# Kernel optimization log

Hardware: AMD Instinct MI355X
Metric: run time of the kernel (lower is better)

The kernel has to match this reference:

```python
import jax, jax.numpy as jnp
import numpy as np

MARGIN = 0.2
LAMBDA_SOFTMAX = 9.0
LAMBDA_LSE = 6.0
WEIGHT_FACTOR = 0.7  # attn_prev is absent/zero on the i2t path
EPS = 1e-8
NEG_INF = -1e9


def setup_inputs() -> dict:
    key = jax.random.key(0)
    k1, k2, k3 = jax.random.split(key, 3)
    B, R, W, D = 128, 36, 32, 256  # batch, regions, max words, feat dim
    im = jax.random.normal(k1, (B, R, D), jnp.float32)
    s = jax.random.normal(k2, (B, W, D), jnp.float32)
    s_l = jax.random.randint(k3, (B,), 1, W + 1)  # caption lengths in [1, W]
    return {"im": im, "s": s, "s_l": s_l}


def _xattn_scores_i2t(im, s, s_l):
    # im: (B, R, D) images; s: (C, W, D) captions; s_l: (C,) lengths
    C, W = s.shape[0], s.shape[1]
    word_mask = jnp.arange(W)[None, :] < s_l[:, None]  # (C, W)

    # func_attention(query=images, context=caption words):
    # attn[c,b,w,r] = <s[c,w], im[b,r]>
    attn = jnp.einsum('cwd,brd->cbwr', s, im)
    # raw_feature_norm == 'clipped_l2norm': LeakyReLU(0.1) then l2norm over region axis
    attn = jax.nn.leaky_relu(attn, 0.1)
    attn = attn / (jnp.sqrt(jnp.sum(attn * attn, axis=-1, keepdims=True)) + EPS)
    # softmax over sourceL = words, with smoothing; mask padded words
    logits = jnp.where(word_mask[:, None, :, None], attn * LAMBDA_SOFTMAX, NEG_INF)
    A = jax.nn.softmax(logits, axis=2)  # (C, B, W, R), sums to 1 over words
    # weightedContext[c,b,r,:] = 0.7 * sum_w A[c,b,w,r] * s[c,w,:]
    wC = WEIGHT_FACTOR * jnp.einsum('cbwr,cwd->cbrd', A, s)

    # cosine similarity between image regions and weighted caption context
    num = jnp.sum(im[None] * wC, axis=-1)                      # (C, B, R)
    denom = jnp.linalg.norm(im, axis=-1)[None] * jnp.linalg.norm(wC, axis=-1)
    row_sim = num / jnp.clip(denom, EPS)

    # agg_func == 'LogSumExp' over regions
    sim = jax.nn.logsumexp(LAMBDA_LSE * row_sim, axis=2) / LAMBDA_LSE  # (C, B)
    return sim.T  # scores: (n_image, n_caption)


def reference(im, s, s_l):
    scores = _xattn_scores_i2t(im, s, s_l)
    diag = jnp.diag(scores)
    cost_s = jnp.clip(MARGIN + scores - diag[:, None], 0.0)   # caption retrieval
    cost_im = jnp.clip(MARGIN + scores - diag[None, :], 0.0)  # image retrieval
    eye = jnp.eye(scores.shape[0], dtype=bool)
    cost_s = jnp.where(eye, 0.0, cost_s)
    cost_im = jnp.where(eye, 0.0, cost_im)
    # max_violation=True: hardest negatives
    return jnp.sum(jnp.max(cost_s, axis=1)) + jnp.sum(jnp.max(cost_im, axis=0))
```

## Files before the change

### kernel.cpp

```cpp
#include <hip/hip_runtime.h>
#include <math.h>

#define CN 128
#define RN 36
#define WN 32
#define DN 256

#define SSTR  264
#define GSTR  40
#define ATSTR 40

#define WS_SCORES 0
#define WS_SF    65536
#define WS_IMF   (WS_SF + CN*16384)
#define WS_TAILF (WS_IMF + CN*16384)
#define WS_G     (WS_TAILF + CN*8192)
#define WS_N2I   (WS_G + CN*2048)
#define WS_NEED  (WS_N2I + CN*RN*4)

typedef unsigned short u16;
typedef __attribute__((ext_vector_type(4))) unsigned short u16x4;
typedef __attribute__((ext_vector_type(8))) unsigned short u16x8;
typedef __attribute__((ext_vector_type(8))) __bf16 bf16x8;
typedef __attribute__((ext_vector_type(4))) float f32x4;

#define C9   12.9842502f
#define C6   8.65616798f
#define IC6  0.115524530f

__device__ __forceinline__ float bf2f(u16 u){ return __uint_as_float(((unsigned)u)<<16); }
__device__ __forceinline__ u16 f2bf(float f){ unsigned x=__float_as_uint(f); return (u16)((x + 0x7fffu + ((x>>16)&1u))>>16); }
__device__ __forceinline__ u16 f2bf_hw(float f){ __bf16 h = (__bf16)f; return __builtin_bit_cast(u16, h); }
__device__ __forceinline__ float lrelu(float v){ return fmaxf(v, 0.1f*v); }

__device__ __forceinline__ void gload16(const void* g, void* l){
    __builtin_amdgcn_global_load_lds((const __attribute__((address_space(1))) void*)g,
                                     (__attribute__((address_space(3))) void*)l, 16, 0, 0);
}

__global__ __launch_bounds__(256)
void precompute_kernel(const float* __restrict__ im, const float* __restrict__ s,
                       char* __restrict__ ws)
{
    const int tid = threadIdx.x;
    if (blockIdx.x < 128) {
        const int i = blockIdx.x;
        __shared__ __align__(16) u16 s_lds[WN*SSTR];
        __shared__ __align__(16) u16 g_lds[WN*GSTR];
        const float* src = s + (size_t)i*(WN*DN);
        u16* outf = (u16*)(ws + WS_SF) + (size_t)i*8192;
#pragma unroll
        for (int it = 0; it < 4; it++) {
            int idx = tid + it*256;
            int m = idx >> 9, ks = (idx >> 6) & 7, ln = idx & 63;
            int cc = ln & 15, gg = ln >> 4;
            const float4* p = (const float4*)(src + (m*16+cc)*DN + ks*32 + gg*8);
            float4 v0 = p[0], v1 = p[1];
            u16x8 hh = { f2bf_hw(v0.x),f2bf_hw(v0.y),f2bf_hw(v0.z),f2bf_hw(v0.w),
                         f2bf_hw(v1.x),f2bf_hw(v1.y),f2bf_hw(v1.z),f2bf_hw(v1.w) };
            *(u16x8*)(outf + (size_t)idx*8) = hh;
            *(u16x8*)&s_lds[(m*16+cc)*SSTR + ks*32 + gg*8] = hh;
        }
        __syncthreads();
        {
            const int lane = tid & 63, wv = tid >> 6;
            const int cc = lane & 15, gg = lane >> 4;
            const int gm = wv >> 1, gn = wv & 1;
            f32x4 acc = {0.f,0.f,0.f,0.f};
#pragma unroll
            for (int ks = 0; ks < 8; ks++) {
                int k0 = ks*32 + gg*8;
                bf16x8 a  = *(const bf16x8*)&s_lds[(gm*16+cc)*SSTR + k0];
                bf16x8 bb = *(const bf16x8*)&s_lds[(gn*16+cc)*SSTR + k0];
                acc = __builtin_amdgcn_mfma_f32_16x16x32_bf16(a, bb, acc, 0, 0, 0);
            }
            u16x4 hg = { f2bf_hw(acc[0]), f2bf_hw(acc[1]), f2bf_hw(acc[2]), f2bf_hw(acc[3]) };
            *(u16x4*)&g_lds[(gn*16+cc)*GSTR + gm*16 + gg*4] = hg;
        }
        __syncthreads();
        if (tid < 128) {
            int t = tid >> 6, ln = tid & 63;
            int cc = ln & 15, gg = ln >> 4;
            u16x8 gv = *(const u16x8*)&g_lds[(t*16+cc)*GSTR + gg*8];
            *(u16x8*)((u16*)(ws + WS_G) + (size_t)i*1024 + tid*8) = gv;
        }
    } else {
        const int i = blockIdx.x - 128;
        const float* src = im + (size_t)i*(RN*DN);
        u16* outf = (u16*)(ws + WS_IMF) + (size_t)i*8192;
#pragma unroll
        for (int it = 0; it < 4; it++) {
            int idx = tid + it*256;
            int m = idx >> 9, ks = (idx >> 6) & 7, ln = idx & 63;
            int cc = ln & 15, gg = ln >> 4;
            const float4* p = (const float4*)(src + (m*16+cc)*DN + ks*32 + gg*8);
            float4 v0 = p[0], v1 = p[1];
            u16x8 hh = { f2bf_hw(v0.x),f2bf_hw(v0.y),f2bf_hw(v0.z),f2bf_hw(v0.w),
                         f2bf_hw(v1.x),f2bf_hw(v1.y),f2bf_hw(v1.z),f2bf_hw(v1.w) };
            *(u16x8*)(outf + (size_t)idx*8) = hh;
        }
        u16* tout = (u16*)(ws + WS_TAILF) + (size_t)i*4096;
#pragma unroll
        for (int it = 0; it < 2; it++) {
            int idx = tid + it*256;
            int ks = idx >> 6, ln = idx & 63;
            int cc = ln & 15, gg = ln >> 4;
            int trow = (cc > 3) ? 3 : cc;
            const float4* p = (const float4*)(src + (32+trow)*DN + ks*32 + gg*8);
            float4 v0 = p[0], v1 = p[1];
            u16x8 hh = { f2bf_hw(v0.x),f2bf_hw(v0.y),f2bf_hw(v0.z),f2bf_hw(v0.w),
                         f2bf_hw(v1.x),f2bf_hw(v1.y),f2bf_hw(v1.z),f2bf_hw(v1.w) };
            *(u16x8*)(tout + (size_t)idx*8) = hh;
        }
        float* n2o = (float*)(ws + WS_N2I) + (size_t)i*RN;
#pragma unroll
        for (int it = 0; it < 2; it++) {
            int idx = tid + it*256;
            if (idx < 288) {
                int r = idx >> 3, q = idx & 7;
                const float4* p = (const float4*)(src + r*DN + q*32);
                float ss = 0.f;
#pragma unroll
                for (int k = 0; k < 8; k++) {
                    float4 v = p[k];
                    ss = fmaf(v.x,v.x,ss); ss = fmaf(v.y,v.y,ss);
                    ss = fmaf(v.z,v.z,ss); ss = fmaf(v.w,v.w,ss);
                }
                ss += __shfl_xor(ss,1); ss += __shfl_xor(ss,2); ss += __shfl_xor(ss,4);
                if (q == 0) n2o[r] = ss;
            }
        }
    }
}

__global__ __launch_bounds__(512, 3)
void xattn_staged(const int* __restrict__ s_l, char* __restrict__ ws)
{
    __shared__ __align__(16) u16 at_all[8*48*ATSTR];

    const int tid = threadIdx.x;
    const int lane = tid & 63, wv = tid >> 6;
    const int bq = blockIdx.x, cp = blockIdx.y;
    const int ci = wv >> 2, bi = wv & 3;
    const int c = cp*2 + ci, b = bq*4 + bi;
    const int col = lane & 15, g4 = lane >> 4;
    const int L = s_l[c];
    const int r2c = (32+col > 35) ? 35 : 32+col;

    const char* sf  = ws + WS_SF    + (size_t)c*16384;
    const char* mf  = ws + WS_IMF   + (size_t)b*16384;
    const char* tf  = ws + WS_TAILF + (size_t)b*8192;
    const char* gfp = ws + WS_G     + (size_t)c*2048;

    bf16x8 gf0 = *(const bf16x8*)(gfp + lane*16);
    bf16x8 gf1 = *(const bf16x8*)(gfp + 1024 + lane*16);
    const float* n2p = (const float*)(ws + WS_N2I) + (size_t)b*RN;
    float n2v0 = n2p[col];
    float n2v1 = n2p[16+col];
    float n2v2 = n2p[r2c];

    f32x4 raw[2][3];
#pragma unroll
    for (int m = 0; m < 2; m++)
#pragma unroll
        for (int n = 0; n < 3; n++) raw[m][n] = (f32x4){0.f,0.f,0.f,0.f};

#pragma unroll
    for (int ks = 0; ks < 8; ks++) {
        bf16x8 a0 = *(const bf16x8*)(sf +        ks*1024 + lane*16);
        bf16x8 a1 = *(const bf16x8*)(sf + 8192 + ks*1024 + lane*16);
        bf16x8 b0 = *(const bf16x8*)(mf +        ks*1024 + lane*16);
        bf16x8 b1 = *(const bf16x8*)(mf + 8192 + ks*1024 + lane*16);
        bf16x8 b2 = *(const bf16x8*)(tf +        ks*1024 + lane*16);
        raw[0][0] = __builtin_amdgcn_mfma_f32_16x16x32_bf16(a0, b0, raw[0][0], 0,0,0);
        raw[0][1] = __builtin_amdgcn_mfma_f32_16x16x32_bf16(a0, b1, raw[0][1], 0,0,0);
        raw[0][2] = __builtin_amdgcn_mfma_f32_16x16x32_bf16(a0, b2, raw[0][2], 0,0,0);
        raw[1][0] = __builtin_amdgcn_mfma_f32_16x16x32_bf16(a1, b0, raw[1][0], 0,0,0);
        raw[1][1] = __builtin_amdgcn_mfma_f32_16x16x32_bf16(a1, b1, raw[1][1], 0,0,0);
        raw[1][2] = __builtin_amdgcn_mfma_f32_16x16x32_bf16(a1, b2, raw[1][2], 0,0,0);
    }

    float af[2][3][4];
#pragma unroll
    for (int m = 0; m < 2; m++) {
#pragma unroll
        for (int reg = 0; reg < 4; reg++) {
            float ssum = 0.f;
#pragma unroll
            for (int n = 0; n < 3; n++) {
                float v = lrelu(raw[m][n][reg]);
                if (n == 2 && col >= 4) v = 0.f;
                af[m][n][reg] = v;
                ssum = fmaf(v, v, ssum);
            }
            ssum += __shfl_xor(ssum, 1);
            ssum += __shfl_xor(ssum, 2);
            ssum += __shfl_xor(ssum, 4);
            ssum += __shfl_xor(ssum, 8);
            float inv2 = C9 / (sqrtf(ssum) + 1e-8f);
#pragma unroll
            for (int n = 0; n < 3; n++) af[m][n][reg] *= inv2;
        }
    }

    float num[3];
#pragma unroll
    for (int n = 0; n < 3; n++) {
        float nm = 0.f;
#pragma unroll
        for (int m = 0; m < 2; m++)
#pragma unroll
            for (int reg = 0; reg < 4; reg++) {
                int w = m*16 + g4*4 + reg;
                float e = (w < L) ? __builtin_amdgcn_exp2f(af[m][n][reg]) : 0.f;
                af[m][n][reg] = e;
                nm = fmaf(e, raw[m][n][reg], nm);
            }
        nm += __shfl_xor(nm, 16);
        nm += __shfl_xor(nm, 32);
        num[n] = nm;
    }

    u16* at = at_all + wv*1920;
#pragma unroll
    for (int m = 0; m < 2; m++)
#pragma unroll
        for (int n = 0; n < 3; n++) {
            u16x4 h = { f2bf_hw(af[m][n][0]), f2bf_hw(af[m][n][1]),
                        f2bf_hw(af[m][n][2]), f2bf_hw(af[m][n][3]) };
            *(u16x4*)&at[(n*16 + col)*ATSTR + m*16 + g4*4] = h;
        }

    float qv[3];
#pragma unroll
    for (int n = 0; n < 3; n++) {
        bf16x8 bfv = *(const bf16x8*)&at[(n*16 + col)*ATSTR + g4*8];
        f32x4 z = {0.f,0.f,0.f,0.f};
        f32x4 t0 = __builtin_amdgcn_mfma_f32_16x16x32_bf16(gf0, bfv, z, 0,0,0);
        f32x4 t1 = __builtin_amdgcn_mfma_f32_16x16x32_bf16(gf1, bfv, z, 0,0,0);
        float q = 0.f;
#pragma unroll
        for (int reg = 0; reg < 4; reg++) {
            q = fmaf(af[0][n][reg], t0[reg], q);
            q = fmaf(af[1][n][reg], t1[reg], q);
        }
        q += __shfl_xor(q, 16);
        q += __shfl_xor(q, 32);
        qv[n] = q;
    }

    float es = 0.f;
#pragma unroll
    for (int n = 0; n < 3; n++) {
        float n2a = (n == 0) ? n2v0 : (n == 1) ? n2v1 : n2v2;
        float rs = num[n] * rsqrtf(fmaxf(n2a * qv[n], 1e-16f));
        bool valid = (n < 2) || (col < 4);
        if (valid) es += __builtin_amdgcn_exp2f(C6 * rs);
    }
    es += __shfl_xor(es, 1);
    es += __shfl_xor(es, 2);
    es += __shfl_xor(es, 4);
    es += __shfl_xor(es, 8);

    if (lane == 0)
        ((float*)(ws + WS_SCORES))[(size_t)b * CN + c] =
            __builtin_amdgcn_logf(es) * IC6;
}

__global__ __launch_bounds__(512, 2)
void xattn_fallback(const float* __restrict__ im, const float* __restrict__ s,
                    const int* __restrict__ s_l, float* __restrict__ scores)
{
    __shared__ u16   s_lds[2][WN*SSTR];
    __shared__ u16   im_lds[4][RN*SSTR];
    __shared__ u16   g_lds[2][WN*GSTR];
    __shared__ u16   at_lds[8][48*ATSTR];
    __shared__ float n2i_lds[4][RN];

    const int tid  = threadIdx.x;
    const int lane = tid & 63;
    const int wv   = tid >> 6;
    const int bq   = blockIdx.x, cp = blockIdx.y;
    const int ci   = wv >> 2, bi = wv & 3;
    const int c    = cp*2 + ci, b = bq*4 + bi;
    const int col  = lane & 15, g4 = lane >> 4;

    if (wv < 4) {
        const float4* g = (const float4*)(im + (size_t)(bq*4 + wv) * (RN*DN));
        u16* dst = im_lds[wv];
#pragma unroll
        for (int k = 0; k < 36; k++) {
            int i = lane + k*64;
            float4 v = g[i];
            int row = i >> 6, cc = (i & 63) * 4;
            u16x4 h = { f2bf(v.x), f2bf(v.y), f2bf(v.z), f2bf(v.w) };
            *(u16x4*)&dst[row*SSTR + cc] = h;
        }
    } else {
        int cap = (wv - 4) >> 1;
        int l2  = ((wv - 4) & 1) * 64 + lane;
        const float4* g = (const float4*)(s + (size_t)(cp*2 + cap) * (WN*DN));
        u16* dst = s_lds[cap];
#pragma unroll
        for (int k = 0; k < 16; k++) {
            int i = l2 + k*128;
            float4 v = g[i];
            int row = i >> 6, cc = (i & 63) * 4;
            u16x4 h = { f2bf(v.x), f2bf(v.y), f2bf(v.z), f2bf(v.w) };
            *(u16x4*)&dst[row*SSTR + cc] = h;
        }
    }
    __syncthreads();

    {
        const int gm = (wv >> 1) & 1, gn = wv & 1;
        const u16* sb = s_lds[ci];
        f32x4 acc = {0.f, 0.f, 0.f, 0.f};
#pragma unroll
        for (int ks = 0; ks < 8; ks++) {
            int k0 = ks*32 + g4*8;
            bf16x8 af = *(const bf16x8*)&sb[(gm*16 + col)*SSTR + k0];
            bf16x8 bfv = *(const bf16x8*)&sb[(gn*16 + col)*SSTR + k0];
            acc = __builtin_amdgcn_mfma_f32_16x16x32_bf16(af, bfv, acc, 0, 0, 0);
        }
        u16x4 h = { f2bf(acc[0]), f2bf(acc[1]), f2bf(acc[2]), f2bf(acc[3]) };
        *(u16x4*)&g_lds[ci][(gn*16 + col)*GSTR + gm*16 + g4*4] = h;
    }

    if (wv < 4) {
        const u16* ib = im_lds[wv];
        int r = lane >> 1, half = lane & 1;
        float ss = 0.f;
        const u16x8* p = (const u16x8*)&ib[r*SSTR + half*128];
#pragma unroll
        for (int k = 0; k < 16; k++) {
            u16x8 v = p[k];
#pragma unroll
            for (int j = 0; j < 8; j++) { float f = bf2f(v[j]); ss = fmaf(f, f, ss); }
        }
        ss += __shfl_xor(ss, 1);
        if (half == 0) n2i_lds[wv][r] = ss;
        if (lane < 8) {
            int r2 = 32 + (lane >> 1), h2 = lane & 1;
            float s2 = 0.f;
            const u16x8* p2 = (const u16x8*)&ib[r2*SSTR + h2*128];
#pragma unroll
            for (int k = 0; k < 16; k++) {
                u16x8 v = p2[k];
#pragma unroll
                for (int j = 0; j < 8; j++) { float f = bf2f(v[j]); s2 = fmaf(f, f, s2); }
            }
            s2 += __shfl_xor(s2, 1);
            if (h2 == 0) n2i_lds[wv][r2] = s2;
        }
    }

    const u16* sb = s_lds[ci];
    const u16* ib = im_lds[bi];
    f32x4 raw[2][3];
#pragma unroll
    for (int m = 0; m < 2; m++)
#pragma unroll
        for (int n = 0; n < 3; n++) raw[m][n] = (f32x4){0.f,0.f,0.f,0.f};
    {
        int r2c = 32 + col; if (r2c > 35) r2c = 35;
#pragma unroll
        for (int ks = 0; ks < 8; ks++) {
            int k0 = ks*32 + g4*8;
            bf16x8 a0 = *(const bf16x8*)&sb[col*SSTR + k0];
            bf16x8 a1 = *(const bf16x8*)&sb[(16 + col)*SSTR + k0];
            bf16x8 b0 = *(const bf16x8*)&ib[col*SSTR + k0];
            bf16x8 b1 = *(const bf16x8*)&ib[(16 + col)*SSTR + k0];
            bf16x8 b2 = *(const bf16x8*)&ib[r2c*SSTR + k0];
            raw[0][0] = __builtin_amdgcn_mfma_f32_16x16x32_bf16(a0, b0, raw[0][0], 0,0,0);
            raw[0][1] = __builtin_amdgcn_mfma_f32_16x16x32_bf16(a0, b1, raw[0][1], 0,0,0);
            raw[0][2] = __builtin_amdgcn_mfma_f32_16x16x32_bf16(a0, b2, raw[0][2], 0,0,0);
            raw[1][0] = __builtin_amdgcn_mfma_f32_16x16x32_bf16(a1, b0, raw[1][0], 0,0,0);
            raw[1][1] = __builtin_amdgcn_mfma_f32_16x16x32_bf16(a1, b1, raw[1][1], 0,0,0);
            raw[1][2] = __builtin_amdgcn_mfma_f32_16x16x32_bf16(a1, b2, raw[1][2], 0,0,0);
        }
    }

    float af[2][3][4];
#pragma unroll
    for (int m = 0; m < 2; m++) {
#pragma unroll
        for (int reg = 0; reg < 4; reg++) {
            float ssum = 0.f;
#pragma unroll
            for (int n = 0; n < 3; n++) {
                float v = lrelu(raw[m][n][reg]);
                if (n == 2 && col >= 4) v = 0.f;
                af[m][n][reg] = v;
                ssum = fmaf(v, v, ssum);
            }
            ssum += __shfl_xor(ssum, 1);
            ssum += __shfl_xor(ssum, 2);
            ssum += __shfl_xor(ssum, 4);
            ssum += __shfl_xor(ssum, 8);
            float inv = 1.0f / (sqrtf(ssum) + 1e-8f);
#pragma unroll
            for (int n = 0; n < 3; n++) af[m][n][reg] *= inv;
        }
    }

    const int L = s_l[c];
    float num[3], qv[3];
#pragma unroll
    for (int n = 0; n < 3; n++) {
        float mx = -1e30f;
#pragma unroll
        for (int m = 0; m < 2; m++)
#pragma unroll
            for (int reg = 0; reg < 4; reg++) {
                int w = m*16 + g4*4 + reg;
                if (w < L) mx = fmaxf(mx, af[m][n][reg]);
            }
        mx = fmaxf(mx, __shfl_xor(mx, 16));
        mx = fmaxf(mx, __shfl_xor(mx, 32));
        mx *= 9.0f;
        float sme = 0.f;
#pragma unroll
        for (int m = 0; m < 2; m++)
#pragma unroll
            for (int reg = 0; reg < 4; reg++) {
                int w = m*16 + g4*4 + reg;
                float e = (w < L) ? __expf(fmaf(9.0f, af[m][n][reg], -mx)) : 0.f;
                af[m][n][reg] = e;
                sme += e;
            }
        sme += __shfl_xor(sme, 16);
        sme += __shfl_xor(sme, 32);
        float inv = 1.0f / sme;
        float nm = 0.f;
#pragma unroll
        for (int m = 0; m < 2; m++)
#pragma unroll
            for (int reg = 0; reg < 4; reg++) {
                af[m][n][reg] *= inv;
                nm = fmaf(af[m][n][reg], raw[m][n][reg], nm);
            }
        nm += __shfl_xor(nm, 16);
        nm += __shfl_xor(nm, 32);
        num[n] = nm;
    }

#pragma unroll
    for (int m = 0; m < 2; m++)
#pragma unroll
        for (int n = 0; n < 3; n++) {
            u16x4 h = { f2bf(af[m][n][0]), f2bf(af[m][n][1]),
                        f2bf(af[m][n][2]), f2bf(af[m][n][3]) };
            *(u16x4*)&at_lds[wv][(n*16 + col)*ATSTR + m*16 + g4*4] = h;
        }

    __syncthreads();

    bf16x8 gf0 = *(const bf16x8*)&g_lds[ci][col*GSTR + g4*8];
    bf16x8 gf1 = *(const bf16x8*)&g_lds[ci][(16+col)*GSTR + g4*8];
    f32x4 tt[2][3];
#pragma unroll
    for (int n = 0; n < 3; n++) {
        bf16x8 bfv = *(const bf16x8*)&at_lds[wv][(n*16 + col)*ATSTR + g4*8];
        f32x4 z = {0.f,0.f,0.f,0.f};
        tt[0][n] = __builtin_amdgcn_mfma_f32_16x16x32_bf16(gf0, bfv, z, 0,0,0);
        tt[1][n] = __builtin_amdgcn_mfma_f32_16x16x32_bf16(gf1, bfv, z, 0,0,0);
    }

#pragma unroll
    for (int n = 0; n < 3; n++) {
        float q = 0.f;
#pragma unroll
        for (int m = 0; m < 2; m++)
#pragma unroll
            for (int reg = 0; reg < 4; reg++) q = fmaf(af[m][n][reg], tt[m][n][reg], q);
        q += __shfl_xor(q, 16);
        q += __shfl_xor(q, 32);
        qv[n] = q;
    }

    float rs[3];
#pragma unroll
    for (int n = 0; n < 3; n++) {
        int r = n*16 + col; if (r > 35) r = 35;
        float n2 = n2i_lds[bi][r];
        float denom = fmaxf(0.7f * sqrtf(n2 * qv[n]), 1e-8f);
        rs[n] = 0.7f * num[n] / denom;
    }
    float xm = -1e30f;
#pragma unroll
    for (int n = 0; n < 3; n++) {
        bool valid = (n < 2) || (col < 4);
        if (valid) xm = fmaxf(xm, 6.0f * rs[n]);
    }
    xm = fmaxf(xm, __shfl_xor(xm, 1));
    xm = fmaxf(xm, __shfl_xor(xm, 2));
    xm = fmaxf(xm, __shfl_xor(xm, 4));
    xm = fmaxf(xm, __shfl_xor(xm, 8));
    float es = 0.f;
#pragma unroll
    for (int n = 0; n < 3; n++) {
        bool valid = (n < 2) || (col < 4);
        if (valid) es += __expf(6.0f * rs[n] - xm);
    }
    es += __shfl_xor(es, 1);
    es += __shfl_xor(es, 2);
    es += __shfl_xor(es, 4);
    es += __shfl_xor(es, 8);

    if (lane == 0) scores[(size_t)b * CN + c] = (xm + __logf(es)) / 6.0f;
}

__global__ __launch_bounds__(1024)
void contrastive_loss_kernel(const float* __restrict__ scores,
                             unsigned int* __restrict__ out)
{
    __shared__ float sc[128][129];
    __shared__ float dg[128];
    __shared__ float red[128];
    const int tid = threadIdx.x;

    const float4* s4 = (const float4*)scores;
#pragma unroll
    for (int it = 0; it < 4; it++) {
        int i = tid + it*1024;
        float4 v = s4[i];
        int row = i >> 5, c4 = (i & 31) << 2;
        sc[row][c4+0] = v.x; sc[row][c4+1] = v.y;
        sc[row][c4+2] = v.z; sc[row][c4+3] = v.w;
    }
    __syncthreads();
    if (tid < 128) dg[tid] = sc[tid][tid];
    __syncthreads();

    const int i = tid >> 3, g = tid & 7;
    const float di = dg[i];
    float rm = 0.f, cm = 0.f;
#pragma unroll
    for (int k = 0; k < 16; k++) {
        int j = g*16 + k;
        if (j != i) {
            rm = fmaxf(rm, 0.2f + sc[i][j] - di);
            cm = fmaxf(cm, 0.2f + sc[j][i] - di);
        }
    }
    rm = fmaxf(rm, __shfl_xor(rm, 1)); cm = fmaxf(cm, __shfl_xor(cm, 1));
    rm = fmaxf(rm, __shfl_xor(rm, 2)); cm = fmaxf(cm, __shfl_xor(cm, 2));
    rm = fmaxf(rm, __shfl_xor(rm, 4)); cm = fmaxf(cm, __shfl_xor(cm, 4));
    if (g == 0) red[i] = rm + cm;
    __syncthreads();

    if (tid < 64) {
        float v = red[tid] + red[tid + 64];
#pragma unroll
        for (int off = 32; off >= 1; off >>= 1) v += __shfl_xor(v, off);
        if (tid == 0) {
            unsigned int x = __float_as_uint(v);
            unsigned int h = (x + 0x7fffu + ((x >> 16) & 1u)) >> 16;
            out[0] = (h << 16) | h;
        }
    }
}

extern "C" void kernel_launch(void* const* d_in, const int* in_sizes, int n_in,
                              void* d_out, int out_size, void* d_ws, size_t ws_size,
                              hipStream_t stream) {
    const float* im  = (const float*)d_in[0];
    const float* s   = (const float*)d_in[1];
    const int*   s_l = (const int*)d_in[2];
    char* ws = (char*)d_ws;

    dim3 grid(32, 64);
    if (ws_size >= (size_t)WS_NEED) {
        precompute_kernel<<<256, 256, 0, stream>>>(im, s, ws);
        xattn_staged<<<grid, 512, 0, stream>>>(s_l, ws);
    } else {
        xattn_fallback<<<grid, 512, 0, stream>>>(im, s, s_l, (float*)ws);
    }
    contrastive_loss_kernel<<<1, 1024, 0, stream>>>((const float*)ws, (unsigned int*)d_out);
}
```

Before: 46.37 us.

## Register-tile 2 captions x 2 images per wave in staged xattn kernel

Each wave now computes a 2x2 block of (caption, image) pairs instead of a single pair. Per k-step it loads 10 fragments to feed 24 MFMAs, where before it loaded 5 fragments per 6 MFMAs, which cuts global/L2 fragment traffic per score. The block shrinks to 256 threads and the grid halves in x. In exchange, each thread holds 24 accumulator vectors, so register use rises and occupancy and latency hiding may drop.

Measured after the change: 77.56 us. +67.2%, slower.

```diff
diff --git a/kernel.cpp b/kernel.cpp
--- a/kernel.cpp
+++ b/kernel.cpp
@@ -133,138 +133,169 @@
     }
 }
 
-__global__ __launch_bounds__(512, 3)
+__global__ __launch_bounds__(256)
 void xattn_staged(const int* __restrict__ s_l, char* __restrict__ ws)
 {
-    __shared__ __align__(16) u16 at_all[8*48*ATSTR];
+    __shared__ __align__(16) u16 at_all[4*48*ATSTR];
 
     const int tid = threadIdx.x;
     const int lane = tid & 63, wv = tid >> 6;
     const int bq = blockIdx.x, cp = blockIdx.y;
-    const int ci = wv >> 2, bi = wv & 3;
-    const int c = cp*2 + ci, b = bq*4 + bi;
+    const int c0 = cp*2;
+    const int b0 = bq*8 + wv*2;
     const int col = lane & 15, g4 = lane >> 4;
-    const int L = s_l[c];
+    const int Lv[2] = { s_l[c0], s_l[c0+1] };
     const int r2c = (32+col > 35) ? 35 : 32+col;
 
-    const char* sf  = ws + WS_SF    + (size_t)c*16384;
-    const char* mf  = ws + WS_IMF   + (size_t)b*16384;
-    const char* tf  = ws + WS_TAILF + (size_t)b*8192;
-    const char* gfp = ws + WS_G     + (size_t)c*2048;
-
-    bf16x8 gf0 = *(const bf16x8*)(gfp + lane*16);
-    bf16x8 gf1 = *(const bf16x8*)(gfp + 1024 + lane*16);
-    const float* n2p = (const float*)(ws + WS_N2I) + (size_t)b*RN;
-    float n2v0 = n2p[col];
-    float n2v1 = n2p[16+col];
-    float n2v2 = n2p[r2c];
-
-    f32x4 raw[2][3];
-#pragma unroll
-    for (int m = 0; m < 2; m++)
-#pragma unroll
-        for (int n = 0; n < 3; n++) raw[m][n] = (f32x4){0.f,0.f,0.f,0.f};
+    const char* sf0 = ws + WS_SF    + (size_t)c0*16384;
+    const char* sf1 = sf0 + 16384;
+    const char* mf0 = ws + WS_IMF   + (size_t)b0*16384;
+    const char* mf1 = mf0 + 16384;
+    const char* tf0 = ws + WS_TAILF + (size_t)b0*8192;
+    const char* tf1 = tf0 + 8192;
+    const char* gfp = ws + WS_G     + (size_t)c0*2048;
+
+    bf16x8 gf[2][2];
+    gf[0][0] = *(const bf16x8*)(gfp +        lane*16);
+    gf[0][1] = *(const bf16x8*)(gfp + 1024 + lane*16);
+    gf[1][0] = *(const bf16x8*)(gfp + 2048 + lane*16);
+    gf[1][1] = *(const bf16x8*)(gfp + 3072 + lane*16);
+    float n2[2][3];
+#pragma unroll
+    for (int img = 0; img < 2; img++) {
+        const float* n2p = (const float*)(ws + WS_N2I) + (size_t)(b0+img)*RN;
+        n2[img][0] = n2p[col];
+        n2[img][1] = n2p[16+col];
+        n2[img][2] = n2p[r2c];
+    }
+
+    f32x4 raw[2][2][2][3];
+#pragma unroll
+    for (int cap = 0; cap < 2; cap++)
+#pragma unroll
+        for (int img = 0; img < 2; img++)
+#pragma unroll
+            for (int m = 0; m < 2; m++)
+#pragma unroll
+                for (int n = 0; n < 3; n++)
+                    raw[cap][img][m][n] = (f32x4){0.f,0.f,0.f,0.f};
 
 #pragma unroll
     for (int ks = 0; ks < 8; ks++) {
-        bf16x8 a0 = *(const bf16x8*)(sf +        ks*1024 + lane*16);
-        bf16x8 a1 = *(const bf16x8*)(sf + 8192 + ks*1024 + lane*16);
-        bf16x8 b0 = *(const bf16x8*)(mf +        ks*1024 + lane*16);
-        bf16x8 b1 = *(const bf16x8*)(mf + 8192 + ks*1024 + lane*16);
-        bf16x8 b2 = *(const bf16x8*)(tf +        ks*1024 + lane*16);
-        raw[0][0] = __builtin_amdgcn_mfma_f32_16x16x32_bf16(a0, b0, raw[0][0], 0,0,0);
-        raw[0][1] = __builtin_amdgcn_mfma_f32_16x16x32_bf16(a0, b1, raw[0][1], 0,0,0);
-        raw[0][2] = __builtin_amdgcn_mfma_f32_16x16x32_bf16(a0, b2, raw[0][2], 0,0,0);
-        raw[1][0] = __builtin_amdgcn_mfma_f32_16x16x32_bf16(a1, b0, raw[1][0], 0,0,0);
-        raw[1][1] = __builtin_amdgcn_mfma_f32_16x16x32_bf16(a1, b1, raw[1][1], 0,0,0);
-        raw[1][2] = __builtin_amdgcn_mfma_f32_16x16x32_bf16(a1, b2, raw[1][2], 0,0,0);
-    }
-
-    float af[2][3][4];
-#pragma unroll
-    for (int m = 0; m < 2; m++) {
-#pragma unroll
-        for (int reg = 0; reg < 4; reg++) {
-            float ssum = 0.f;
+        bf16x8 a[2][2], bb[2][3];
+        a[0][0]  = *(const bf16x8*)(sf0 +        ks*1024 + lane*16);
+        a[0][1]  = *(const bf16x8*)(sf0 + 8192 + ks*1024 + lane*16);
+        a[1][0]  = *(const bf16x8*)(sf1 +        ks*1024 + lane*16);
+        a[1][1]  = *(const bf16x8*)(sf1 + 8192 + ks*1024 + lane*16);
+        bb[0][0] = *(const bf16x8*)(mf0 +        ks*1024 + lane*16);
+        bb[0][1] = *(const bf16x8*)(mf0 + 8192 + ks*1024 + lane*16);
+        bb[0][2] = *(const bf16x8*)(tf0 +        ks*1024 + lane*16);
+        bb[1][0] = *(const bf16x8*)(mf1 +        ks*1024 + lane*16);
+        bb[1][1] = *(const bf16x8*)(mf1 + 8192 + ks*1024 + lane*16);
+        bb[1][2] = *(const bf16x8*)(tf1 +        ks*1024 + lane*16);
+#pragma unroll
+        for (int cap = 0; cap < 2; cap++)
+#pragma unroll
+            for (int img = 0; img < 2; img++)
+#pragma unroll
+                for (int m = 0; m < 2; m++)
+#pragma unroll
+                    for (int n = 0; n < 3; n++)
+                        raw[cap][img][m][n] = __builtin_amdgcn_mfma_f32_16x16x32_bf16(
+                            a[cap][m], bb[img][n], raw[cap][img][m][n], 0,0,0);
+    }
+
+    u16* at = at_all + wv*1920;
+#pragma unroll
+    for (int cap = 0; cap < 2; cap++) {
+#pragma unroll
+        for (int img = 0; img < 2; img++) {
+            float af[2][3][4];
+#pragma unroll
+            for (int m = 0; m < 2; m++) {
+#pragma unroll
+                for (int reg = 0; reg < 4; reg++) {
+                    float ssum = 0.f;
+#pragma unroll
+                    for (int n = 0; n < 3; n++) {
+                        float v = lrelu(raw[cap][img][m][n][reg]);
+                        if (n == 2 && col >= 4) v = 0.f;
+                        af[m][n][reg] = v;
+                        ssum = fmaf(v, v, ssum);
+                    }
+                    ssum += __shfl_xor(ssum, 1);
+                    ssum += __shfl_xor(ssum, 2);
+                    ssum += __shfl_xor(ssum, 4);
+                    ssum += __shfl_xor(ssum, 8);
+                    float inv2 = C9 / (sqrtf(ssum) + 1e-8f);
+#pragma unroll
+                    for (int n = 0; n < 3; n++) af[m][n][reg] *= inv2;
+                }
+            }
+
+            const int L = Lv[cap];
+            float num[3];
 #pragma unroll
             for (int n = 0; n < 3; n++) {
-                float v = lrelu(raw[m][n][reg]);
-                if (n == 2 && col >= 4) v = 0.f;
-                af[m][n][reg] = v;
-                ssum = fmaf(v, v, ssum);
-            }
-            ssum += __shfl_xor(ssum, 1);
-            ssum += __shfl_xor(ssum, 2);
-            ssum += __shfl_xor(ssum, 4);
-            ssum += __shfl_xor(ssum, 8);
-            float inv2 = C9 / (sqrtf(ssum) + 1e-8f);
-#pragma unroll
-            for (int n = 0; n < 3; n++) af[m][n][reg] *= inv2;
-        }
-    }
-
-    float num[3];
-#pragma unroll
-    for (int n = 0; n < 3; n++) {
-        float nm = 0.f;
-#pragma unroll
-        for (int m = 0; m < 2; m++)
-#pragma unroll
-            for (int reg = 0; reg < 4; reg++) {
-                int w = m*16 + g4*4 + reg;
-                float e = (w < L) ? __builtin_amdgcn_exp2f(af[m][n][reg]) : 0.f;
-                af[m][n][reg] = e;
-                nm = fmaf(e, raw[m][n][reg], nm);
-            }
-        nm += __shfl_xor(nm, 16);
-        nm += __shfl_xor(nm, 32);
-        num[n] = nm;
-    }
-
-    u16* at = at_all + wv*1920;
-#pragma unroll
-    for (int m = 0; m < 2; m++)
-#pragma unroll
-        for (int n = 0; n < 3; n++) {
-            u16x4 h = { f2bf_hw(af[m][n][0]), f2bf_hw(af[m][n][1]),
-                        f2bf_hw(af[m][n][2]), f2bf_hw(af[m][n][3]) };
-            *(u16x4*)&at[(n*16 + col)*ATSTR + m*16 + g4*4] = h;
-        }
-
-    float qv[3];
-#pragma unroll
-    for (int n = 0; n < 3; n++) {
-        bf16x8 bfv = *(const bf16x8*)&at[(n*16 + col)*ATSTR + g4*8];
-        f32x4 z = {0.f,0.f,0.f,0.f};
-        f32x4 t0 = __builtin_amdgcn_mfma_f32_16x16x32_bf16(gf0, bfv, z, 0,0,0);
-        f32x4 t1 = __builtin_amdgcn_mfma_f32_16x16x32_bf16(gf1, bfv, z, 0,0,0);
-        float q = 0.f;
-#pragma unroll
-        for (int reg = 0; reg < 4; reg++) {
-            q = fmaf(af[0][n][reg], t0[reg], q);
-            q = fmaf(af[1][n][reg], t1[reg], q);
-        }
-        q += __shfl_xor(q, 16);
-        q += __shfl_xor(q, 32);
-        qv[n] = q;
-    }
-
-    float es = 0.f;
-#pragma unroll
-    for (int n = 0; n < 3; n++) {
-        float n2a = (n == 0) ? n2v0 : (n == 1) ? n2v1 : n2v2;
-        float rs = num[n] * rsqrtf(fmaxf(n2a * qv[n], 1e-16f));
-        bool valid = (n < 2) || (col < 4);
-        if (valid) es += __builtin_amdgcn_exp2f(C6 * rs);
-    }
-    es += __shfl_xor(es, 1);
-    es += __shfl_xor(es, 2);
-    es += __shfl_xor(es, 4);
-    es += __shfl_xor(es, 8);
-
-    if (lane == 0)
-        ((float*)(ws + WS_SCORES))[(size_t)b * CN + c] =
-            __builtin_amdgcn_logf(es) * IC6;
+                float nm = 0.f;
+#pragma unroll
+                for (int m = 0; m < 2; m++)
+#pragma unroll
+                    for (int reg = 0; reg < 4; reg++) {
+                        int w = m*16 + g4*4 + reg;
+                        float e = (w < L) ? __builtin_amdgcn_exp2f(af[m][n][reg]) : 0.f;
+                        af[m][n][reg] = e;
+                        nm = fmaf(e, raw[cap][img][m][n][reg], nm);
+                    }
+                nm += __shfl_xor(nm, 16);
+                nm += __shfl_xor(nm, 32);
+                num[n] = nm;
+            }
+
+#pragma unroll
+            for (int m = 0; m < 2; m++)
+#pragma unroll
+                for (int n = 0; n < 3; n++) {
+                    u16x4 h = { f2bf_hw(af[m][n][0]), f2bf_hw(af[m][n][1]),
+                                f2bf_hw(af[m][n][2]), f2bf_hw(af[m][n][3]) };
+                    *(u16x4*)&at[(n*16 + col)*ATSTR + m*16 + g4*4] = h;
+                }
+
+            float qv[3];
+#pragma unroll
+            for (int n = 0; n < 3; n++) {
+                bf16x8 bfv = *(const bf16x8*)&at[(n*16 + col)*ATSTR + g4*8];
+                f32x4 z = {0.f,0.f,0.f,0.f};
+                f32x4 t0 = __builtin_amdgcn_mfma_f32_16x16x32_bf16(gf[cap][0], bfv, z, 0,0,0);
+                f32x4 t1 = __builtin_amdgcn_mfma_f32_16x16x32_bf16(gf[cap][1], bfv, z, 0,0,0);
+                float q = 0.f;
+#pragma unroll
+                for (int reg = 0; reg < 4; reg++) {
+                    q = fmaf(af[0][n][reg], t0[reg], q);
+                    q = fmaf(af[1][n][reg], t1[reg], q);
+                }
+                q += __shfl_xor(q, 16);
+                q += __shfl_xor(q, 32);
+                qv[n] = q;
+            }
+
+            float es = 0.f;
+#pragma unroll
+            for (int n = 0; n < 3; n++) {
+                float rs = num[n] * rsqrtf(fmaxf(n2[img][n] * qv[n], 1e-16f));
+                bool valid = (n < 2) || (col < 4);
+                if (valid) es += __builtin_amdgcn_exp2f(C6 * rs);
+            }
+            es += __shfl_xor(es, 1);
+            es += __shfl_xor(es, 2);
+            es += __shfl_xor(es, 4);
+            es += __shfl_xor(es, 8);
+
+            if (lane == 0)
+                ((float*)(ws + WS_SCORES))[(size_t)(b0+img) * CN + (c0+cap)] =
+                    __builtin_amdgcn_logf(es) * IC6;
+        }
+    }
 }
 
 __global__ __launch_bounds__(512, 2)
@@ -570,11 +601,12 @@
     const int*   s_l = (const int*)d_in[2];
     char* ws = (char*)d_ws;
 
-    dim3 grid(32, 64);
     if (ws_size >= (size_t)WS_NEED) {
         precompute_kernel<<<256, 256, 0, stream>>>(im, s, ws);
-        xattn_staged<<<grid, 512, 0, stream>>>(s_l, ws);
+        dim3 grid(16, 64);
+        xattn_staged<<<grid, 256, 0, stream>>>(s_l, ws);
     } else {
+        dim3 grid(32, 64);
         xattn_fallback<<<grid, 512, 0, stream>>>(im, s, s_l, (float*)ws);
     }
     contrastive_loss_kernel<<<1, 1024, 0, stream>>>((const float*)ws, (unsigned int*)d_out);
```
